# Kernel optimization log

Measured on AMD Instinct MI355X. Metric: run time of the kernel, lower is better.

The kernel has to match this reference:

```python
import jax, jax.numpy as jnp
import numpy as np

B, CIN, H, W = 1, 512, 128, 128
NC, D, P, NH = 10, 128, 200, 8
HW = H * W
DH = D // NH
FF = 256


def setup_inputs():
    key = jax.random.key(0)
    ks = jax.random.split(key, 20)
    def nrm(i, shape, s=0.02):
        return jax.random.normal(ks[i], shape, jnp.float32) * s
    # TransFusion create_2D_grid: pixel-center coords (x, y), flattened to [1, HW, 2]
    xs = jnp.arange(W, dtype=jnp.float32) + 0.5
    ys = jnp.arange(H, dtype=jnp.float32) + 0.5
    gx, gy = jnp.meshgrid(xs, ys, indexing='xy')
    bev_pos = jnp.stack([gx.reshape(-1), gy.reshape(-1)], axis=-1)[None]
    return {
        'x': jax.random.normal(ks[0], (B, CIN, H, W), jnp.float32),
        'w_shared': nrm(1, (D, CIN, 3, 3)), 'b_shared': jnp.zeros((D,), jnp.float32),
        'w_heat': nrm(2, (NC, D, 3, 3)), 'b_heat': jnp.full((NC,), -2.19, jnp.float32),
        'classes_eye': jnp.eye(NC, dtype=jnp.float32),
        'bev_pos': bev_pos,
        'w_ce': nrm(3, (D, NC)), 'b_ce': jnp.zeros((D,), jnp.float32),
        'w_qpos': nrm(4, (D, 2)), 'w_kpos': nrm(5, (D, 2)),
        'wq': nrm(6, (D, D)), 'wk': nrm(7, (D, D)), 'wv': nrm(8, (D, D)), 'wo': nrm(9, (D, D)),
        'ln1_g': jnp.ones((D,), jnp.float32), 'ln1_b': jnp.zeros((D,), jnp.float32),
        'ln2_g': jnp.ones((D,), jnp.float32), 'ln2_b': jnp.zeros((D,), jnp.float32),
        'w_ff1': nrm(10, (FF, D)), 'b_ff1': jnp.zeros((FF,), jnp.float32),
        'w_ff2': nrm(11, (D, FF)), 'b_ff2': jnp.zeros((D,), jnp.float32),
        'w_center': nrm(12, (2, D)), 'b_center': jnp.zeros((2,), jnp.float32),
        'w_height': nrm(13, (1, D)), 'b_height': jnp.zeros((1,), jnp.float32),
        'w_dim': nrm(14, (3, D)), 'b_dim': jnp.zeros((3,), jnp.float32),
        'w_rot': nrm(15, (2, D)), 'b_rot': jnp.zeros((2,), jnp.float32),
        'w_vel': nrm(16, (2, D)), 'b_vel': jnp.zeros((2,), jnp.float32),
        'w_hm': nrm(17, (NC, D)), 'b_hm': jnp.zeros((NC,), jnp.float32),
    }


def _conv2d(x, w, b):
    y = jax.lax.conv_general_dilated(x, w, (1, 1), 'SAME',
                                     dimension_numbers=('NCHW', 'OIHW', 'NCHW'))
    return y + b[None, :, None, None]


def _ln(x, g, b):
    m = jnp.mean(x, -1, keepdims=True)
    v = jnp.var(x, -1, keepdims=True)
    return (x - m) * jax.lax.rsqrt(v + 1e-5) * g + b


def reference(x, w_shared, b_shared, w_heat, b_heat, classes_eye, bev_pos,
              w_ce, b_ce, w_qpos, w_kpos, wq, wk, wv, wo,
              ln1_g, ln1_b, ln2_g, ln2_b, w_ff1, b_ff1, w_ff2, b_ff2,
              w_center, b_center, w_height, b_height, w_dim, b_dim,
              w_rot, b_rot, w_vel, b_vel, w_hm, b_hm):
    lidar_feat = jax.nn.relu(_conv2d(x, w_shared, b_shared))          # [B,D,H,W]
    lidar_flat = lidar_feat.reshape(B, D, HW)
    dense_heatmap = _conv2d(lidar_feat, w_heat, b_heat)               # [B,NC,H,W]
    heatmap = jax.lax.stop_gradient(jax.nn.sigmoid(dense_heatmap))    # .detach().sigmoid()
    # 3x3 local-max 'NMS'; zero-initialized border (F.max_pool2d VALID placed into zeros)
    inner = jax.lax.reduce_window(heatmap, -jnp.inf, jax.lax.max,
                                  (1, 1, 3, 3), (1, 1, 1, 1), 'VALID')
    local_max = jnp.zeros_like(heatmap).at[:, :, 1:-1, 1:-1].set(inner)
    local_max = local_max.at[:, 8].set(heatmap[:, 8])  # nuScenes: no NMS for cls 8,9
    local_max = local_max.at[:, 9].set(heatmap[:, 9])
    heatmap = heatmap * (heatmap == local_max)
    hm_flat = heatmap.reshape(B, NC, HW)
    # top-k proposals over flattened class*position axis
    _, top = jax.lax.top_k(hm_flat.reshape(B, -1), P)
    top_cls = top // HW                                               # [B,P]
    top_idx = top % HW                                                # [B,P]
    query_feat = jnp.take_along_axis(
        lidar_flat, jnp.broadcast_to(top_idx[:, None, :], (B, D, P)), axis=2)
    one_hot = classes_eye[top_cls].transpose(0, 2, 1)                 # [B,NC,P]
    # class encoding: 1x1 conv1d on one-hot
    query_feat = query_feat + jnp.einsum('dc,bcp->bdp', w_ce, one_hot) + b_ce[None, :, None]
    query_pos = jnp.take_along_axis(
        jnp.broadcast_to(bev_pos, (B, HW, 2)),
        jnp.broadcast_to(top_idx[:, :, None], (B, P, 2)), axis=1)     # [B,P,2]
    # single decoder layer: cross-attention of proposals over BEV features
    q_in = query_feat.transpose(0, 2, 1) + query_pos @ w_qpos.T       # [B,P,D]
    kv_in = lidar_flat.transpose(0, 2, 1) + bev_pos @ w_kpos.T        # [B,HW,D]
    q = (q_in @ wq.T).reshape(B, P, NH, DH)
    k = (kv_in @ wk.T).reshape(B, HW, NH, DH)
    v = (kv_in @ wv.T).reshape(B, HW, NH, DH)
    attn = jax.nn.softmax(jnp.einsum('bqhd,bkhd->bhqk', q, k) / np.sqrt(DH).astype(np.float32), axis=-1)
    out = jnp.einsum('bhqk,bkhd->bqhd', attn, v).reshape(B, P, D) @ wo.T
    h1 = _ln(query_feat.transpose(0, 2, 1) + out, ln1_g, ln1_b)
    ff = jax.nn.relu(h1 @ w_ff1.T + b_ff1) @ w_ff2.T + b_ff2
    h2 = _ln(h1 + ff, ln2_g, ln2_b)
    feat = h2.transpose(0, 2, 1)                                      # [B,D,P]
    def head(wt, bt):
        return jnp.einsum('od,bdp->bop', wt, feat) + bt[None, :, None]
    center = head(w_center, b_center) + query_pos.transpose(0, 2, 1)
    height = head(w_height, b_height)
    dim = head(w_dim, b_dim)
    rot = head(w_rot, b_rot)
    vel = head(w_vel, b_vel)
    hm_pred = head(w_hm, b_hm)
    query_heatmap_score = jnp.take_along_axis(
        hm_flat, jnp.broadcast_to(top_idx[:, None, :], (B, NC, P)), axis=2)
    # get_bboxes: sigmoid(heatmap) * query_heatmap_score * one_hot
    score = jax.nn.sigmoid(hm_pred) * query_heatmap_score * one_hot
    return (score, rot, dim, center, height, vel)
```

## Files before the change

### kernel.cpp

```cpp
#include <hip/hip_runtime.h>
#include <math.h>

#define HWSZ 16384

typedef __attribute__((ext_vector_type(8))) short short8;
typedef __attribute__((ext_vector_type(8))) unsigned short ush8;
typedef __attribute__((ext_vector_type(4))) float f4;
typedef __attribute__((ext_vector_type(16))) float f16x;

__device__ __forceinline__ ushort f2bf(float f) {
    unsigned u = __float_as_uint(f);
    return (ushort)((u + 0x7fffu + ((u >> 16) & 1u)) >> 16);
}
__device__ __forceinline__ float bf2f(ushort b) {
    return __uint_as_float(((unsigned)b) << 16);
}

__global__ void k_prep_w2(const float* __restrict__ w, float* __restrict__ wt) {
    int idx = blockIdx.x * 256 + threadIdx.x;
    if (idx >= 1152 * 16) return;
    int k = idx >> 4, oc = idx & 15;
    wt[idx] = (oc < 10) ? w[oc * 1152 + k] : 0.f;
}
__global__ void k_cvt_w(const float* __restrict__ w, ushort* __restrict__ wh,
                        ushort* __restrict__ wl) {
    int idx = blockIdx.x * 256 + threadIdx.x;
    if (idx >= 589824) return;
    int oc = idx / 4608, r = idx - oc * 4608;
    int tap = r >> 9, c = r & 511;
    float f = w[oc * 4608 + c * 9 + tap];
    ushort hb = f2bf(f);
    wh[idx] = hb;
    wl[idx] = f2bf(f - bf2f(hb));
}
__global__ void k_cvt_w128(const float* __restrict__ a, const float* __restrict__ b,
                           ushort* __restrict__ oa, ushort* __restrict__ ob) {
    int i = blockIdx.x * 256 + threadIdx.x;
    if (i < 16384) { oa[i] = f2bf(a[i]); ob[i] = f2bf(b[i]); }
}
__global__ __launch_bounds__(256) void k_cvt_x(const float* __restrict__ x,
        ushort* __restrict__ xh, ushort* __restrict__ xl) {
    __shared__ float T[64 * 65];
    int hw0 = blockIdx.x << 6;
    int c0 = blockIdx.y << 6;
    int t = threadIdx.x;
    {
        int cl = t >> 2, q = t & 3;
        const float* src = x + (size_t)(c0 + cl) * HWSZ + hw0 + q * 16;
        #pragma unroll
        for (int k = 0; k < 4; k++) {
            float4 v = *reinterpret_cast<const float4*>(src + k * 4);
            float* dst = &T[cl * 65 + q * 16 + k * 4];
            dst[0] = v.x; dst[1] = v.y; dst[2] = v.z; dst[3] = v.w;
        }
    }
    __syncthreads();
    {
        int hwl = t >> 2, q = t & 3;
        int cc = q * 16;
        size_t ob = (size_t)(hw0 + hwl) * 512 + c0 + cc;
        #pragma unroll
        for (int half = 0; half < 2; half++) {
            ush8 hv, lv;
            #pragma unroll
            for (int k = 0; k < 8; k++) {
                float f = T[(cc + half * 8 + k) * 65 + hwl];
                ushort hb = f2bf(f);
                hv[k] = hb;
                lv[k] = f2bf(f - bf2f(hb));
            }
            *reinterpret_cast<ush8*>(xh + ob + half * 8) = hv;
            *reinterpret_cast<ush8*>(xl + ob + half * 8) = lv;
        }
    }
}

__global__ __launch_bounds__(256) void k_conv1_mfma(
        const ushort* __restrict__ xh, const ushort* __restrict__ xl,
        const ushort* __restrict__ wh, const ushort* __restrict__ wl,
        const float* __restrict__ bias, float* __restrict__ out) {
    __shared__ ushort smem[30720];
    const int t = threadIdx.x;
    const int h = blockIdx.x >> 1, w0 = (blockIdx.x & 1) << 6;
    const int l = t & 63;
    const int wid = t >> 6;
    const int wm = wid >> 1, wn = wid & 1;
    const int l15 = l & 15, lhi = l >> 4;
    const int arow = t >> 2, achk = t & 3;

    f4 acc[2][4];
    #pragma unroll
    for (int m = 0; m < 2; m++)
        #pragma unroll
        for (int n = 0; n < 4; n++) acc[m][n] = (f4){0.f, 0.f, 0.f, 0.f};

    short8 rA[2], rB[2][2];
    const short8 zz = {0, 0, 0, 0, 0, 0, 0, 0};

    auto issue = [&](int it) {
        int c0 = (it / 9) << 5;
        int tap = it % 9;
        int dh = tap / 3 - 1, dw = tap % 3 - 1;
        int hh = h + dh;
        int wg = w0 + arow + dw;
        if (hh >= 0 && hh < 128 && wg >= 0 && wg < 128) {
            size_t off = ((size_t)(hh * 128 + wg) << 9) + c0 + (achk << 3);
            rA[0] = *reinterpret_cast<const short8*>(xh + off);
            rA[1] = *reinterpret_cast<const short8*>(xl + off);
        } else { rA[0] = zz; rA[1] = zz; }
        #pragma unroll
        for (int u = 0; u < 2; u++) {
            int oc = (u << 6) + (t >> 2);
            size_t off = (size_t)oc * 4608 + tap * 512 + c0 + (achk << 3);
            rB[u][0] = *reinterpret_cast<const short8*>(wh + off);
            rB[u][1] = *reinterpret_cast<const short8*>(wl + off);
        }
    };
    auto wstage = [&](int buf) {
        *reinterpret_cast<short8*>(&smem[buf * 5120 + arow * 40 + achk * 8]) = rA[0];
        *reinterpret_cast<short8*>(&smem[buf * 5120 + 2560 + arow * 40 + achk * 8]) = rA[1];
        #pragma unroll
        for (int u = 0; u < 2; u++) {
            int oc = (u << 6) + (t >> 2);
            *reinterpret_cast<short8*>(&smem[10240 + buf * 10240 + oc * 40 + achk * 8]) = rB[u][0];
            *reinterpret_cast<short8*>(&smem[10240 + buf * 10240 + 5120 + oc * 40 + achk * 8]) = rB[u][1];
        }
    };

    issue(0);
    wstage(0);
    issue(1);
    __syncthreads();

    for (int it = 0; it < 144; ++it) {
        int buf = it & 1;
        short8 aH[2], aL[2], bH[4], bL[4];
        #pragma unroll
        for (int m = 0; m < 2; m++) {
            int row = wm * 32 + m * 16 + l15;
            aH[m] = *reinterpret_cast<const short8*>(&smem[buf * 5120 + row * 40 + lhi * 8]);
            aL[m] = *reinterpret_cast<const short8*>(&smem[buf * 5120 + 2560 + row * 40 + lhi * 8]);
        }
        #pragma unroll
        for (int n = 0; n < 4; n++) {
            int oc = wn * 64 + n * 16 + l15;
            bH[n] = *reinterpret_cast<const short8*>(&smem[10240 + buf * 10240 + oc * 40 + lhi * 8]);
            bL[n] = *reinterpret_cast<const short8*>(&smem[10240 + buf * 10240 + 5120 + oc * 40 + lhi * 8]);
        }
        #pragma unroll
        for (int m = 0; m < 2; m++)
            #pragma unroll
            for (int n = 0; n < 4; n++) {
                acc[m][n] = __builtin_amdgcn_mfma_f32_16x16x32_bf16(aH[m], bH[n], acc[m][n], 0, 0, 0);
                acc[m][n] = __builtin_amdgcn_mfma_f32_16x16x32_bf16(aL[m], bH[n], acc[m][n], 0, 0, 0);
                acc[m][n] = __builtin_amdgcn_mfma_f32_16x16x32_bf16(aH[m], bL[n], acc[m][n], 0, 0, 0);
            }
        if (it + 1 < 144) {
            wstage(buf ^ 1);
            if (it + 2 < 144) issue(it + 2);
        }
        __syncthreads();
    }

    float* ot = reinterpret_cast<float*>(smem);
    #pragma unroll
    for (int m = 0; m < 2; m++)
        #pragma unroll
        for (int n = 0; n < 4; n++) {
            int oc = wn * 64 + n * 16 + l15;
            float b = bias[oc];
            #pragma unroll
            for (int r = 0; r < 4; r++) {
                int px = wm * 32 + m * 16 + lhi * 4 + r;
                ot[px * 132 + oc] = fmaxf(acc[m][n][r] + b, 0.f);
            }
        }
    __syncthreads();
    {
        int oc = t >> 1, half = t & 1;
        int base = h * 128 + w0 + half * 32;
        #pragma unroll
        for (int i = 0; i < 32; i += 4) {
            float4 v;
            v.x = ot[(half * 32 + i + 0) * 132 + oc];
            v.y = ot[(half * 32 + i + 1) * 132 + oc];
            v.z = ot[(half * 32 + i + 2) * 132 + oc];
            v.w = ot[(half * 32 + i + 3) * 132 + oc];
            *reinterpret_cast<float4*>(&out[(size_t)oc * HWSZ + base + i]) = v;
        }
    }
}

__global__ __launch_bounds__(256) void k_conv2(const float* __restrict__ lidar,
        const float* __restrict__ wt, const float* __restrict__ bias,
        float* __restrict__ sig) {
    __shared__ float xs[16 * 3 * 68];
    __shared__ float wsm[144 * 16];
    int bid = blockIdx.x;
    int h = bid >> 1, w0 = (bid & 1) << 6;
    int t = threadIdx.x;
    int tpx = (t & 15) << 2;
    int oc = t >> 4;
    float acc[4] = {0.f, 0.f, 0.f, 0.f};
    for (int c0 = 0; c0 < 128; c0 += 16) {
        for (int i = t; i < 16 * 3 * 66; i += 256) {
            int c = i / 198; int rem = i - c * 198; int r = rem / 66; int j = rem - r * 66;
            int gr = h - 1 + r, gc = w0 - 1 + j;
            float v = 0.f;
            if (((unsigned)gr < 128u) & ((unsigned)gc < 128u))
                v = lidar[(c0 + c) * HWSZ + gr * 128 + gc];
            xs[(c * 3 + r) * 68 + j] = v;
        }
        {
            const float4* src = (const float4*)(wt + c0 * 9 * 16);
            float4* dst = (float4*)wsm;
            for (int i = t; i < 576; i += 256) dst[i] = src[i];
        }
        __syncthreads();
        #pragma unroll 4
        for (int c = 0; c < 16; c++) {
            #pragma unroll
            for (int kh = 0; kh < 3; kh++) {
                const float* xr = &xs[(c * 3 + kh) * 68 + tpx];
                float xv0 = xr[0], xv1 = xr[1], xv2 = xr[2], xv3 = xr[3], xv4 = xr[4], xv5 = xr[5];
                #pragma unroll
                for (int kw = 0; kw < 3; kw++) {
                    float wv = wsm[(c * 9 + kh * 3 + kw) * 16 + oc];
                    float p0 = (kw == 0) ? xv0 : ((kw == 1) ? xv1 : xv2);
                    float p1 = (kw == 0) ? xv1 : ((kw == 1) ? xv2 : xv3);
                    float p2 = (kw == 0) ? xv2 : ((kw == 1) ? xv3 : xv4);
                    float p3 = (kw == 0) ? xv3 : ((kw == 1) ? xv4 : xv5);
                    acc[0] += p0 * wv; acc[1] += p1 * wv; acc[2] += p2 * wv; acc[3] += p3 * wv;
                }
            }
        }
        __syncthreads();
    }
    if (oc < 10) {
        float b = bias[oc];
        int col = h * 128 + w0 + tpx;
        float4 v;
        v.x = 1.f / (1.f + expf(-(acc[0] + b)));
        v.y = 1.f / (1.f + expf(-(acc[1] + b)));
        v.z = 1.f / (1.f + expf(-(acc[2] + b)));
        v.w = 1.f / (1.f + expf(-(acc[3] + b)));
        *(float4*)&sig[oc * HWSZ + col] = v;
    }
}

__global__ void k_nms(const float* __restrict__ sig, float* __restrict__ hm) {
    int gid = blockIdx.x * 256 + threadIdx.x;
    int c = gid >> 14, i = gid & 16383;
    int h = i >> 7, w = i & 127;
    float v = sig[gid];
    float keep = 0.f;
    if (c >= 8) keep = v;
    else if (h >= 1 && h <= 126 && w >= 1 && w <= 126) {
        const float* s = sig + c * HWSZ;
        float m = v;
        #pragma unroll
        for (int dh = -1; dh <= 1; dh++)
            #pragma unroll
            for (int dw = -1; dw <= 1; dw++)
                m = fmaxf(m, s[(h + dh) * 128 + (w + dw)]);
        keep = (v == m) ? v : 0.f;
    }
    hm[gid] = keep;
}

__global__ void k_hist_hi(const float* __restrict__ hm, unsigned* __restrict__ hist) {
    int gid = blockIdx.x * 256 + threadIdx.x;
    unsigned k = __float_as_uint(hm[gid]);
    if (k) atomicAdd(&hist[k >> 16], 1u);
}
__global__ void k_scan_hi(const unsigned* __restrict__ hist, unsigned* __restrict__ state) {
    __shared__ unsigned ps[256];
    __shared__ int selc;
    __shared__ unsigned selcum;
    __shared__ unsigned cb[256];
    int t = threadIdx.x;
    unsigned s = 0;
    const unsigned* hp = hist + t * 256;
    for (int i = 0; i < 256; i++) s += hp[i];
    ps[t] = s;
    __syncthreads();
    if (t == 0) {
        unsigned cum = 0; int c = 255;
        for (; c > 0; c--) { if (cum + ps[c] >= 200u) break; cum += ps[c]; }
        selc = c; selcum = cum;
    }
    __syncthreads();
    int c = selc;
    cb[t] = hist[c * 256 + t];
    __syncthreads();
    if (t == 0) {
        unsigned cum = selcum; int b = 255;
        for (; b > 0; b--) { if (cum + cb[b] >= 200u) break; cum += cb[b]; }
        state[8] = (unsigned)(c * 256 + b);
        state[9] = 200u - cum;
        state[10] = cum;
    }
}
__global__ void k_hist_lo(const float* __restrict__ hm, const unsigned* __restrict__ state,
                          unsigned* __restrict__ hist) {
    int gid = blockIdx.x * 256 + threadIdx.x;
    unsigned k = __float_as_uint(hm[gid]);
    if (k && (k >> 16) == state[8]) atomicAdd(&hist[k & 0xFFFFu], 1u);
}
__global__ void k_scan_lo(const unsigned* __restrict__ hist, unsigned* __restrict__ state) {
    __shared__ unsigned ps[256];
    __shared__ int selc;
    __shared__ unsigned selcum;
    __shared__ unsigned cb[256];
    int t = threadIdx.x;
    unsigned target = state[9];
    unsigned s = 0;
    const unsigned* hp = hist + t * 256;
    for (int i = 0; i < 256; i++) s += hp[i];
    ps[t] = s;
    __syncthreads();
    if (t == 0) {
        unsigned cum = 0; int c = 255;
        for (; c > 0; c--) { if (cum + ps[c] >= target) break; cum += ps[c]; }
        selc = c; selcum = cum;
    }
    __syncthreads();
    int c = selc;
    cb[t] = hist[c * 256 + t];
    __syncthreads();
    if (t == 0) {
        unsigned cum = selcum; int b = 255;
        for (; b > 0; b--) { if (cum + cb[b] >= target) break; cum += cb[b]; }
        unsigned lstar = (unsigned)(c * 256 + b);
        state[2] = (state[8] << 16) | lstar;
        state[0] = state[10] + cum;
        state[1] = target - cum;
    }
}
__global__ void k_collect(const float* __restrict__ hm, const unsigned* __restrict__ state,
        unsigned* __restrict__ ck, unsigned* __restrict__ ci,
        unsigned* __restrict__ ti, unsigned* __restrict__ cnts) {
    int gid = blockIdx.x * 256 + threadIdx.x;
    unsigned k = __float_as_uint(hm[gid]);
    unsigned ks = state[2];
    if (k > ks) {
        unsigned pos = atomicAdd(&cnts[0], 1u);
        if (pos < 256u) { ck[pos] = k; ci[pos] = (unsigned)gid; }
    } else if (k == ks) {
        unsigned pos = atomicAdd(&cnts[1], 1u);
        if (pos < 8192u) ti[pos] = (unsigned)gid;
    }
}
__global__ void k_topk_final(const unsigned* __restrict__ state, const unsigned* __restrict__ cnts,
        const unsigned* __restrict__ ck, const unsigned* __restrict__ ci,
        const unsigned* __restrict__ ti, int* __restrict__ top_pos, int* __restrict__ top_cls) {
    __shared__ unsigned kk[200], ii[200];
    int t = threadIdx.x;
    unsigned cgt = cnts[0];
    unsigned need = state[1];
    unsigned keystar = state[2];
    unsigned cntEq = cnts[1]; if (cntEq > 8192u) cntEq = 8192u;
    if ((unsigned)t < cgt && t < 200) { kk[t] = ck[t]; ii[t] = ci[t]; }
    for (unsigned e = t; e < cntEq; e += 256) {
        unsigned my = ti[e]; unsigned r = 0;
        for (unsigned j = 0; j < cntEq; j++) r += (ti[j] < my);
        if (r < need) { kk[cgt + r] = keystar; ii[cgt + r] = my; }
    }
    __syncthreads();
    if (t < 200) {
        unsigned mk = kk[t], mi = ii[t]; int r = 0;
        for (int j = 0; j < 200; j++) {
            unsigned ok = kk[j], oi = ii[j];
            r += (ok > mk) || (ok == mk && oi < mi);
        }
        top_cls[r] = (int)(mi >> 14);
        top_pos[r] = (int)(mi & 16383u);
    }
}

__global__ void k_gather(const float* __restrict__ lidar, const int* __restrict__ top_pos,
        const int* __restrict__ top_cls, const float* __restrict__ w_ce,
        const float* __restrict__ b_ce, const float* __restrict__ w_qpos,
        float* __restrict__ qf, float* __restrict__ qin, float* __restrict__ qpos) {
    int gid = blockIdx.x * 256 + threadIdx.x;
    if (gid >= 200 * 128) return;
    int p = gid >> 7, d = gid & 127;
    int idx = top_pos[p], cls = top_cls[p];
    float px = (float)(idx & 127) + 0.5f, py = (float)(idx >> 7) + 0.5f;
    float v = lidar[d * HWSZ + idx] + w_ce[d * 10 + cls] + b_ce[d];
    qf[gid] = v;
    qin[gid] = v + px * w_qpos[d * 2] + py * w_qpos[d * 2 + 1];
    if (d < 2) qpos[p * 2 + d] = (d == 0) ? px : py;
}

__global__ __launch_bounds__(256) void k_kvin(const float* __restrict__ lidar,
        const float* __restrict__ w_kpos, ushort* __restrict__ kv) {
    __shared__ float T[128 * 65];
    int hw0 = blockIdx.x << 6;
    int t = threadIdx.x;
    for (int i = t; i < 128 * 64; i += 256) {
        int d = i >> 6, c = i & 63;
        T[d * 65 + c] = lidar[d * HWSZ + hw0 + c];
    }
    __syncthreads();
    for (int i = t; i < 64 * 128; i += 256) {
        int r = i >> 7, d = i & 127;
        int hw = hw0 + r;
        float bx = (float)(hw & 127) + 0.5f, by = (float)(hw >> 7) + 0.5f;
        kv[(size_t)hw * 128 + d] = f2bf(T[d * 65 + r] + bx * w_kpos[d * 2] + by * w_kpos[d * 2 + 1]);
    }
}

__global__ __launch_bounds__(256) void k_gemm_kv(const ushort* __restrict__ A,
        const ushort* __restrict__ B, float* __restrict__ C) {
    __shared__ ushort As[64 * 136];
    __shared__ ushort Bs[128 * 136];
    int m0 = blockIdx.x << 6;
    int t = threadIdx.x;
    {
        int r = t >> 3, c = (t & 7) << 4;
        #pragma unroll
        for (int p = 0; p < 2; p++) {
            int row = p * 32 + r;
            const ush8* src = reinterpret_cast<const ush8*>(A + (size_t)(m0 + row) * 128 + c);
            *reinterpret_cast<ush8*>(&As[row * 136 + c]) = src[0];
            *reinterpret_cast<ush8*>(&As[row * 136 + c + 8]) = src[1];
        }
        #pragma unroll
        for (int p = 0; p < 4; p++) {
            int row = p * 32 + r;
            const ush8* src = reinterpret_cast<const ush8*>(B + (size_t)row * 128 + c);
            *reinterpret_cast<ush8*>(&Bs[row * 136 + c]) = src[0];
            *reinterpret_cast<ush8*>(&Bs[row * 136 + c + 8]) = src[1];
        }
    }
    __syncthreads();
    int l = t & 63, wid = t >> 6;
    int wm = wid >> 1, wn = wid & 1;
    int l31 = l & 31, lk = l >> 5;
    f16x acc[2];
    #pragma unroll
    for (int n = 0; n < 2; n++)
        #pragma unroll
        for (int i = 0; i < 16; i++) acc[n][i] = 0.f;
    #pragma unroll
    for (int ks = 0; ks < 8; ks++) {
        short8 aF = *reinterpret_cast<const short8*>(&As[(wm * 32 + l31) * 136 + ks * 16 + lk * 8]);
        #pragma unroll
        for (int n = 0; n < 2; n++) {
            short8 bF = *reinterpret_cast<const short8*>(&Bs[(wn * 64 + n * 32 + l31) * 136 + ks * 16 + lk * 8]);
            acc[n] = __builtin_amdgcn_mfma_f32_32x32x16_bf16(aF, bF, acc[n], 0, 0, 0);
        }
    }
    #pragma unroll
    for (int n = 0; n < 2; n++) {
        int oc = wn * 64 + n * 32 + l31;
        size_t cb = (size_t)(oc >> 4) * HWSZ * 16 + (oc & 15);
        #pragma unroll
        for (int r = 0; r < 16; r++) {
            int mrow = wm * 32 + (r & 3) + ((r >> 2) << 3) + (lk << 2);
            C[cb + (size_t)(m0 + mrow) * 16] = acc[n][r];
        }
    }
}

template<int EPI>
__global__ __launch_bounds__(256) void k_gemm(const float* __restrict__ A,
        const float* __restrict__ B, float* __restrict__ C, int M, int N, int K,
        const float* __restrict__ bias, const float* __restrict__ res) {
    __shared__ float As[16 * 68];
    __shared__ float Bs[16 * 68];
    int m0 = blockIdx.x * 64, n0 = blockIdx.y * 64;
    int t = threadIdx.x;
    int mi = (t & 15) << 2, ni = (t >> 4) << 2;
    float acc[4][4];
    #pragma unroll
    for (int i = 0; i < 4; i++)
        #pragma unroll
        for (int j = 0; j < 4; j++) acc[i][j] = 0.f;
    int r = t >> 2, kq = (t & 3) << 2;
    for (int k0 = 0; k0 < K; k0 += 16) {
        float4 v = make_float4(0.f, 0.f, 0.f, 0.f);
        if (m0 + r < M) v = *(const float4*)&A[(m0 + r) * K + k0 + kq];
        As[(kq + 0) * 68 + r] = v.x; As[(kq + 1) * 68 + r] = v.y;
        As[(kq + 2) * 68 + r] = v.z; As[(kq + 3) * 68 + r] = v.w;
        float4 w = *(const float4*)&B[(n0 + r) * K + k0 + kq];
        Bs[(kq + 0) * 68 + r] = w.x; Bs[(kq + 1) * 68 + r] = w.y;
        Bs[(kq + 2) * 68 + r] = w.z; Bs[(kq + 3) * 68 + r] = w.w;
        __syncthreads();
        #pragma unroll
        for (int k = 0; k < 16; k++) {
            float4 a = *(const float4*)&As[k * 68 + mi];
            float4 b = *(const float4*)&Bs[k * 68 + ni];
            acc[0][0] += a.x * b.x; acc[0][1] += a.x * b.y; acc[0][2] += a.x * b.z; acc[0][3] += a.x * b.w;
            acc[1][0] += a.y * b.x; acc[1][1] += a.y * b.y; acc[1][2] += a.y * b.z; acc[1][3] += a.y * b.w;
            acc[2][0] += a.z * b.x; acc[2][1] += a.z * b.y; acc[2][2] += a.z * b.z; acc[2][3] += a.z * b.w;
            acc[3][0] += a.w * b.x; acc[3][1] += a.w * b.y; acc[3][2] += a.w * b.z; acc[3][3] += a.w * b.w;
        }
        __syncthreads();
    }
    #pragma unroll
    for (int i = 0; i < 4; i++) {
        int m = m0 + mi + i;
        if (m >= M) continue;
        #pragma unroll
        for (int j = 0; j < 4; j++) {
            int n = n0 + ni + j;
            float v = acc[i][j];
            if (EPI == 2) v = fmaxf(v + bias[n], 0.f);
            if (EPI == 3) v += bias[n] + res[m * N + n];
            C[m * N + n] = v;
        }
    }
}

__global__ __launch_bounds__(256, 1) void k_attn_part(const float* __restrict__ Q,
        const float* __restrict__ Kp, const float* __restrict__ Vp,
        float* __restrict__ ps, float* __restrict__ pacc) {
    int head = blockIdx.y, chunk = blockIdx.z;
    int t = threadIdx.x;
    int wv = t >> 6, lane = t & 63;
    int qbase = (blockIdx.x * 4 + wv) * 4;
    float q[4][16];
    #pragma unroll
    for (int qq = 0; qq < 4; qq++) {
        int p = qbase + qq; if (p > 199) p = 199;
        const float4* qr = (const float4*)(Q + p * 128 + head * 16);
        #pragma unroll
        for (int u = 0; u < 4; u++) {
            float4 v = qr[u];
            q[qq][u * 4 + 0] = v.x * 0.25f; q[qq][u * 4 + 1] = v.y * 0.25f;
            q[qq][u * 4 + 2] = v.z * 0.25f; q[qq][u * 4 + 3] = v.w * 0.25f;
        }
    }
    const float* Kh = Kp + (size_t)head * HWSZ * 16;
    const float* Vh = Vp + (size_t)head * HWSZ * 16;
    float s[4] = {0.f, 0.f, 0.f, 0.f};
    float acc[4][16];
    #pragma unroll
    for (int qq = 0; qq < 4; qq++)
        #pragma unroll
        for (int i = 0; i < 16; i++) acc[qq][i] = 0.f;
    int k0 = chunk << 10;
    for (int kb = k0 + lane; kb < k0 + 1024; kb += 64) {
        const float4* kr = (const float4*)(Kh + (size_t)kb * 16);
        float4 ka = kr[0], kb4 = kr[1], kc = kr[2], kd = kr[3];
        float kk[16] = {ka.x, ka.y, ka.z, ka.w, kb4.x, kb4.y, kb4.z, kb4.w,
                        kc.x, kc.y, kc.z, kc.w, kd.x, kd.y, kd.z, kd.w};
        const float4* vr = (const float4*)(Vh + (size_t)kb * 16);
        float4 va = vr[0], vb = vr[1], vc = vr[2], vd = vr[3];
        float vv[16] = {va.x, va.y, va.z, va.w, vb.x, vb.y, vb.z, vb.w,
                        vc.x, vc.y, vc.z, vc.w, vd.x, vd.y, vd.z, vd.w};
        #pragma unroll
        for (int qq = 0; qq < 4; qq++) {
            float l0 = fmaf(q[qq][3], kk[3], fmaf(q[qq][2], kk[2], fmaf(q[qq][1], kk[1], q[qq][0] * kk[0])));
            float l1 = fmaf(q[qq][7], kk[7], fmaf(q[qq][6], kk[6], fmaf(q[qq][5], kk[5], q[qq][4] * kk[4])));
            float l2 = fmaf(q[qq][11], kk[11], fmaf(q[qq][10], kk[10], fmaf(q[qq][9], kk[9], q[qq][8] * kk[8])));
            float l3 = fmaf(q[qq][15], kk[15], fmaf(q[qq][14], kk[14], fmaf(q[qq][13], kk[13], q[qq][12] * kk[12])));
            float e = __expf((l0 + l1) + (l2 + l3));
            s[qq] += e;
            #pragma unroll
            for (int i = 0; i < 16; i++) acc[qq][i] = fmaf(e, vv[i], acc[qq][i]);
        }
    }
    #pragma unroll
    for (int mask = 32; mask >= 1; mask >>= 1) {
        #pragma unroll
        for (int qq = 0; qq < 4; qq++) {
            s[qq] += __shfl_xor(s[qq], mask);
            #pragma unroll
            for (int i = 0; i < 16; i++) acc[qq][i] += __shfl_xor(acc[qq][i], mask);
        }
    }
    if (lane == 0) {
        #pragma unroll
        for (int qq = 0; qq < 4; qq++) {
            int p = qbase + qq;
            int idx = (chunk * 8 + head) * 208 + p;
            ps[idx] = s[qq];
            #pragma unroll
            for (int i = 0; i < 16; i++) pacc[idx * 16 + i] = acc[qq][i];
        }
    }
}
__global__ __launch_bounds__(128) void k_attn_comb(const float* __restrict__ ps,
        const float* __restrict__ pacc, float* __restrict__ out) {
    int p = blockIdx.x;
    int t = threadIdx.x;
    int h = t >> 4, d = t & 15;
    float S = 0.f, A = 0.f;
    #pragma unroll
    for (int c = 0; c < 16; c++) {
        int idx = (c * 8 + h) * 208 + p;
        S += ps[idx];
        A += pacc[idx * 16 + d];
    }
    out[p * 128 + h * 16 + d] = A / S;
}

__global__ void k_ln(const float* __restrict__ a, const float* __restrict__ b,
        const float* __restrict__ g, const float* __restrict__ be, float* __restrict__ out) {
    int p = blockIdx.x, d = threadIdx.x;
    float x = a[p * 128 + d];
    if (b) x += b[p * 128 + d];
    __shared__ float red[4];
    float s = x;
    #pragma unroll
    for (int mask = 32; mask >= 1; mask >>= 1) s += __shfl_xor(s, mask);
    if ((d & 63) == 0) red[d >> 6] = s;
    __syncthreads();
    float mean = (red[0] + red[1]) * (1.f / 128.f);
    float dx = x - mean;
    float s2 = dx * dx;
    #pragma unroll
    for (int mask = 32; mask >= 1; mask >>= 1) s2 += __shfl_xor(s2, mask);
    if ((d & 63) == 0) red[2 + (d >> 6)] = s2;
    __syncthreads();
    float var = (red[2] + red[3]) * (1.f / 128.f);
    out[p * 128 + d] = dx * rsqrtf(var + 1e-5f) * g[d] + be[d];
}

__global__ void k_heads(const float* __restrict__ h2, const float* __restrict__ hm,
        const int* __restrict__ top_pos, const int* __restrict__ top_cls,
        const float* __restrict__ qpos,
        const float* __restrict__ w_hm, const float* __restrict__ b_hm,
        const float* __restrict__ w_rot, const float* __restrict__ b_rot,
        const float* __restrict__ w_dim, const float* __restrict__ b_dim,
        const float* __restrict__ w_center, const float* __restrict__ b_center,
        const float* __restrict__ w_height, const float* __restrict__ b_height,
        const float* __restrict__ w_vel, const float* __restrict__ b_vel,
        float* __restrict__ out) {
    int gid = blockIdx.x * 256 + threadIdx.x;
    if (gid >= 4000) return;
    int o = gid / 200, p = gid - o * 200;
    const float* wr; float bias;
    if (o < 10)      { wr = w_hm + o * 128;            bias = b_hm[o]; }
    else if (o < 12) { wr = w_rot + (o - 10) * 128;    bias = b_rot[o - 10]; }
    else if (o < 15) { wr = w_dim + (o - 12) * 128;    bias = b_dim[o - 12]; }
    else if (o < 17) { wr = w_center + (o - 15) * 128; bias = b_center[o - 15]; }
    else if (o < 18) { wr = w_height;                  bias = b_height[0]; }
    else             { wr = w_vel + (o - 18) * 128;    bias = b_vel[o - 18]; }
    const float* hr = h2 + p * 128;
    float dot = 0.f;
    #pragma unroll 8
    for (int d = 0; d < 128; d++) dot = fmaf(wr[d], hr[d], dot);
    dot += bias;
    float outv; int off;
    if (o < 10) {
        float qhs = hm[o * HWSZ + top_pos[p]];
        float oh = (top_cls[p] == o) ? 1.f : 0.f;
        outv = (1.f / (1.f + expf(-dot))) * qhs * oh;
        off = o * 200 + p;
    } else if (o < 12) { outv = dot; off = 2000 + (o - 10) * 200 + p; }
    else if (o < 15)   { outv = dot; off = 2400 + (o - 12) * 200 + p; }
    else if (o < 17)   { outv = dot + qpos[p * 2 + (o - 15)]; off = 3000 + (o - 15) * 200 + p; }
    else if (o < 18)   { outv = dot; off = 3400 + p; }
    else               { outv = dot; off = 3600 + (o - 18) * 200 + p; }
    out[off] = outv;
}

extern "C" void kernel_launch(void* const* d_in, const int* in_sizes, int n_in,
                              void* d_out, int out_size, void* d_ws, size_t ws_size,
                              hipStream_t stream) {
    const float* x        = (const float*)d_in[0];
    const float* w_shared = (const float*)d_in[1];
    const float* b_shared = (const float*)d_in[2];
    const float* w_heat   = (const float*)d_in[3];
    const float* b_heat   = (const float*)d_in[4];
    const float* w_ce     = (const float*)d_in[7];
    const float* b_ce     = (const float*)d_in[8];
    const float* w_qpos   = (const float*)d_in[9];
    const float* w_kpos   = (const float*)d_in[10];
    const float* wq       = (const float*)d_in[11];
    const float* wk       = (const float*)d_in[12];
    const float* wv       = (const float*)d_in[13];
    const float* wo       = (const float*)d_in[14];
    const float* ln1_g    = (const float*)d_in[15];
    const float* ln1_b    = (const float*)d_in[16];
    const float* ln2_g    = (const float*)d_in[17];
    const float* ln2_b    = (const float*)d_in[18];
    const float* w_ff1    = (const float*)d_in[19];
    const float* b_ff1    = (const float*)d_in[20];
    const float* w_ff2    = (const float*)d_in[21];
    const float* b_ff2    = (const float*)d_in[22];
    const float* w_center = (const float*)d_in[23];
    const float* b_center = (const float*)d_in[24];
    const float* w_height = (const float*)d_in[25];
    const float* b_height = (const float*)d_in[26];
    const float* w_dim    = (const float*)d_in[27];
    const float* b_dim    = (const float*)d_in[28];
    const float* w_rot    = (const float*)d_in[29];
    const float* b_rot    = (const float*)d_in[30];
    const float* w_vel    = (const float*)d_in[31];
    const float* b_vel    = (const float*)d_in[32];
    const float* w_hm     = (const float*)d_in[33];
    const float* b_hm     = (const float*)d_in[34];
    float* out = (float*)d_out;

    float* ws = (float*)d_ws;
    float* lidar = ws;
    float* bigR  = lidar + 2097152;
    ushort* xt_hi = (ushort*)bigR;
    ushort* xt_lo = xt_hi + 8388608;
    ushort* kvb  = (ushort*)bigR;
    float* KpB   = bigR + 2097152;
    float* VpB   = bigR + 4194304;
    float* wbh_f = bigR + 8388608;
    float* wbl_f = wbh_f + 294912;
    ushort* wb_hi = (ushort*)wbh_f;
    ushort* wb_lo = (ushort*)wbl_f;
    float* wt2   = wbl_f + 294912;
    float* sig   = wt2 + 18432;
    float* hmb   = sig + 163840;
    unsigned* hist_hi = (unsigned*)(hmb + 163840);
    unsigned* hist_lo = hist_hi + 65536;
    unsigned* state   = hist_lo + 65536;
    unsigned* cnts    = state + 64;
    unsigned* ck      = cnts + 64;
    unsigned* ci      = ck + 256;
    unsigned* ti      = ci + 256;
    int* top_pos      = (int*)(ti + 8192);
    int* top_cls      = top_pos + 256;
    float* qpos  = (float*)(top_cls + 256);
    float* qf    = qpos + 512;
    float* qin   = qf + 25600;
    float* qbuf  = qin + 25600;
    float* attno = qbuf + 25600;
    float* wo_o  = attno + 25600;
    float* h1    = wo_o + 25600;
    float* f1    = h1 + 25600;
    float* ff2o  = f1 + 51200;
    float* h2    = ff2o + 25600;
    float* ps_b  = h2 + 25600;
    float* pacc_b = ps_b + 26624;
    ushort* wkb  = (ushort*)(pacc_b + 425984);
    ushort* wvb  = wkb + 16384;
    size_t needed = (size_t)((pacc_b + 425984 + 16384) - ws) * sizeof(float);
    if (ws_size < needed) return;

    k_prep_w2<<<72, 256, 0, stream>>>(w_heat, wt2);
    k_cvt_w<<<2304, 256, 0, stream>>>(w_shared, wb_hi, wb_lo);
    k_cvt_w128<<<64, 256, 0, stream>>>(wk, wv, wkb, wvb);
    k_cvt_x<<<dim3(256, 8), 256, 0, stream>>>(x, xt_hi, xt_lo);
    k_conv1_mfma<<<256, 256, 0, stream>>>(xt_hi, xt_lo, wb_hi, wb_lo, b_shared, lidar);
    k_conv2<<<256, 256, 0, stream>>>(lidar, wt2, b_heat, sig);
    k_nms<<<640, 256, 0, stream>>>(sig, hmb);
    hipMemsetAsync(hist_hi, 0, (65536u * 2 + 128) * sizeof(unsigned), stream);
    k_hist_hi<<<640, 256, 0, stream>>>(hmb, hist_hi);
    k_scan_hi<<<1, 256, 0, stream>>>(hist_hi, state);
    k_hist_lo<<<640, 256, 0, stream>>>(hmb, state, hist_lo);
    k_scan_lo<<<1, 256, 0, stream>>>(hist_lo, state);
    k_collect<<<640, 256, 0, stream>>>(hmb, state, ck, ci, ti, cnts);
    k_topk_final<<<1, 256, 0, stream>>>(state, cnts, ck, ci, ti, top_pos, top_cls);
    k_gather<<<100, 256, 0, stream>>>(lidar, top_pos, top_cls, w_ce, b_ce, w_qpos, qf, qin, qpos);
    k_kvin<<<256, 256, 0, stream>>>(lidar, w_kpos, kvb);
    k_gemm<0><<<dim3(4, 2), 256, 0, stream>>>(qin, wq, qbuf, 200, 128, 128, nullptr, nullptr);
    k_gemm_kv<<<256, 256, 0, stream>>>(kvb, wkb, KpB);
    k_gemm_kv<<<256, 256, 0, stream>>>(kvb, wvb, VpB);
    k_attn_part<<<dim3(13, 8, 16), 256, 0, stream>>>(qbuf, KpB, VpB, ps_b, pacc_b);
    k_attn_comb<<<200, 128, 0, stream>>>(ps_b, pacc_b, attno);
    k_gemm<0><<<dim3(4, 2), 256, 0, stream>>>(attno, wo, wo_o, 200, 128, 128, nullptr, nullptr);
    k_ln<<<200, 128, 0, stream>>>(qf, wo_o, ln1_g, ln1_b, h1);
    k_gemm<2><<<dim3(4, 4), 256, 0, stream>>>(h1, w_ff1, f1, 200, 256, 128, b_ff1, nullptr);
    k_gemm<3><<<dim3(4, 2), 256, 0, stream>>>(f1, w_ff2, ff2o, 200, 128, 256, b_ff2, h1);
    k_ln<<<200, 128, 0, stream>>>(ff2o, nullptr, ln2_g, ln2_b, h2);
    k_heads<<<16, 256, 0, stream>>>(h2, hmb, top_pos, top_cls, qpos,
        w_hm, b_hm, w_rot, b_rot, w_dim, b_dim, w_center, b_center,
        w_height, b_height, w_vel, b_vel, out);
}
```

Measured before the change: 528.1 us.

## Fuse histogram into NMS, store K/V in bf16, fuse transformer tail

Three changes. The high-bits histogram atomics move into the NMS kernel, which drops one launch and one full reread of the heatmap. The K/V projection outputs are stored as bf16 instead of fp32, halving the bytes the attention kernel streams, at some precision cost. The Wo projection, LN1, FFN and LN2 are merged into one per-query kernel, replacing five small launches and their intermediate buffers with serial per-thread dot products.

```diff
diff --git a/kernel.cpp b/kernel.cpp
--- a/kernel.cpp
+++ b/kernel.cpp
@@ -248,7 +248,8 @@
     }
 }
 
-__global__ void k_nms(const float* __restrict__ sig, float* __restrict__ hm) {
+__global__ void k_nms(const float* __restrict__ sig, float* __restrict__ hm,
+                      unsigned* __restrict__ hist) {
     int gid = blockIdx.x * 256 + threadIdx.x;
     int c = gid >> 14, i = gid & 16383;
     int h = i >> 7, w = i & 127;
@@ -266,13 +267,10 @@
         keep = (v == m) ? v : 0.f;
     }
     hm[gid] = keep;
-}
-
-__global__ void k_hist_hi(const float* __restrict__ hm, unsigned* __restrict__ hist) {
-    int gid = blockIdx.x * 256 + threadIdx.x;
-    unsigned k = __float_as_uint(hm[gid]);
-    if (k) atomicAdd(&hist[k >> 16], 1u);
-}
+    unsigned kb = __float_as_uint(keep);
+    if (kb) atomicAdd(&hist[kb >> 16], 1u);
+}
+
 __global__ void k_scan_hi(const unsigned* __restrict__ hist, unsigned* __restrict__ state) {
     __shared__ unsigned ps[256];
     __shared__ int selc;
@@ -412,7 +410,7 @@
 }
 
 __global__ __launch_bounds__(256) void k_gemm_kv(const ushort* __restrict__ A,
-        const ushort* __restrict__ B, float* __restrict__ C) {
+        const ushort* __restrict__ B, ushort* __restrict__ C) {
     __shared__ ushort As[64 * 136];
     __shared__ ushort Bs[128 * 136];
     int m0 = blockIdx.x << 6;
@@ -459,7 +457,7 @@
         #pragma unroll
         for (int r = 0; r < 16; r++) {
             int mrow = wm * 32 + (r & 3) + ((r >> 2) << 3) + (lk << 2);
-            C[cb + (size_t)(m0 + mrow) * 16] = acc[n][r];
+            C[cb + (size_t)(m0 + mrow) * 16] = f2bf(acc[n][r]);
         }
     }
 }
@@ -515,7 +513,7 @@
 }
 
 __global__ __launch_bounds__(256, 1) void k_attn_part(const float* __restrict__ Q,
-        const float* __restrict__ Kp, const float* __restrict__ Vp,
+        const ushort* __restrict__ Kp, const ushort* __restrict__ Vp,
         float* __restrict__ ps, float* __restrict__ pacc) {
     int head = blockIdx.y, chunk = blockIdx.z;
     int t = threadIdx.x;
@@ -533,8 +531,8 @@
             q[qq][u * 4 + 2] = v.z * 0.25f; q[qq][u * 4 + 3] = v.w * 0.25f;
         }
     }
-    const float* Kh = Kp + (size_t)head * HWSZ * 16;
-    const float* Vh = Vp + (size_t)head * HWSZ * 16;
+    const ushort* Kh = Kp + (size_t)head * HWSZ * 16;
+    const ushort* Vh = Vp + (size_t)head * HWSZ * 16;
     float s[4] = {0.f, 0.f, 0.f, 0.f};
     float acc[4][16];
     #pragma unroll
@@ -543,14 +541,16 @@
         for (int i = 0; i < 16; i++) acc[qq][i] = 0.f;
     int k0 = chunk << 10;
     for (int kb = k0 + lane; kb < k0 + 1024; kb += 64) {
-        const float4* kr = (const float4*)(Kh + (size_t)kb * 16);
-        float4 ka = kr[0], kb4 = kr[1], kc = kr[2], kd = kr[3];
-        float kk[16] = {ka.x, ka.y, ka.z, ka.w, kb4.x, kb4.y, kb4.z, kb4.w,
-                        kc.x, kc.y, kc.z, kc.w, kd.x, kd.y, kd.z, kd.w};
-        const float4* vr = (const float4*)(Vh + (size_t)kb * 16);
-        float4 va = vr[0], vb = vr[1], vc = vr[2], vd = vr[3];
-        float vv[16] = {va.x, va.y, va.z, va.w, vb.x, vb.y, vb.z, vb.w,
-                        vc.x, vc.y, vc.z, vc.w, vd.x, vd.y, vd.z, vd.w};
+        const ush8* kr = reinterpret_cast<const ush8*>(Kh + (size_t)kb * 16);
+        ush8 kA = kr[0], kB = kr[1];
+        const ush8* vr = reinterpret_cast<const ush8*>(Vh + (size_t)kb * 16);
+        ush8 vA = vr[0], vB = vr[1];
+        float kk[16], vv[16];
+        #pragma unroll
+        for (int i = 0; i < 8; i++) {
+            kk[i] = bf2f(kA[i]); kk[8 + i] = bf2f(kB[i]);
+            vv[i] = bf2f(vA[i]); vv[8 + i] = bf2f(vB[i]);
+        }
         #pragma unroll
         for (int qq = 0; qq < 4; qq++) {
             float l0 = fmaf(q[qq][3], kk[3], fmaf(q[qq][2], kk[2], fmaf(q[qq][1], kk[1], q[qq][0] * kk[0])));
@@ -598,12 +598,22 @@
     out[p * 128 + h * 16 + d] = A / S;
 }
 
-__global__ void k_ln(const float* __restrict__ a, const float* __restrict__ b,
-        const float* __restrict__ g, const float* __restrict__ be, float* __restrict__ out) {
+__global__ __launch_bounds__(128) void k_tail(const float* __restrict__ attno,
+        const float* __restrict__ qf, const float* __restrict__ wo,
+        const float* __restrict__ ln1_g, const float* __restrict__ ln1_b,
+        const float* __restrict__ w_ff1, const float* __restrict__ b_ff1,
+        const float* __restrict__ w_ff2, const float* __restrict__ b_ff2,
+        const float* __restrict__ ln2_g, const float* __restrict__ ln2_b,
+        float* __restrict__ h2out) {
     int p = blockIdx.x, d = threadIdx.x;
-    float x = a[p * 128 + d];
-    if (b) x += b[p * 128 + d];
-    __shared__ float red[4];
+    __shared__ float att[128], h1s[128], fs[256], red[4];
+    att[d] = attno[p * 128 + d];
+    __syncthreads();
+    float acc = 0.f;
+    const float* wr = wo + d * 128;
+    #pragma unroll 8
+    for (int k = 0; k < 128; k++) acc = fmaf(wr[k], att[k], acc);
+    float x = qf[p * 128 + d] + acc;
     float s = x;
     #pragma unroll
     for (int mask = 32; mask >= 1; mask >>= 1) s += __shfl_xor(s, mask);
@@ -617,7 +627,41 @@
     if ((d & 63) == 0) red[2 + (d >> 6)] = s2;
     __syncthreads();
     float var = (red[2] + red[3]) * (1.f / 128.f);
-    out[p * 128 + d] = dx * rsqrtf(var + 1e-5f) * g[d] + be[d];
+    float h1v = dx * rsqrtf(var + 1e-5f) * ln1_g[d] + ln1_b[d];
+    h1s[d] = h1v;
+    __syncthreads();
+    float a0 = 0.f, a1 = 0.f;
+    const float* w1a = w_ff1 + d * 128;
+    const float* w1b = w_ff1 + (d + 128) * 128;
+    #pragma unroll 8
+    for (int k = 0; k < 128; k++) {
+        float hv = h1s[k];
+        a0 = fmaf(w1a[k], hv, a0);
+        a1 = fmaf(w1b[k], hv, a1);
+    }
+    fs[d] = fmaxf(a0 + b_ff1[d], 0.f);
+    fs[d + 128] = fmaxf(a1 + b_ff1[d + 128], 0.f);
+    __syncthreads();
+    float a2 = 0.f;
+    const float* w2 = w_ff2 + d * 256;
+    #pragma unroll 8
+    for (int j = 0; j < 256; j++) a2 = fmaf(w2[j], fs[j], a2);
+    float x2 = h1v + a2 + b_ff2[d];
+    __syncthreads();
+    float t2 = x2;
+    #pragma unroll
+    for (int mask = 32; mask >= 1; mask >>= 1) t2 += __shfl_xor(t2, mask);
+    if ((d & 63) == 0) red[d >> 6] = t2;
+    __syncthreads();
+    float mean2 = (red[0] + red[1]) * (1.f / 128.f);
+    float dx2 = x2 - mean2;
+    float v2 = dx2 * dx2;
+    #pragma unroll
+    for (int mask = 32; mask >= 1; mask >>= 1) v2 += __shfl_xor(v2, mask);
+    if ((d & 63) == 0) red[2 + (d >> 6)] = v2;
+    __syncthreads();
+    float var2 = (red[2] + red[3]) * (1.f / 128.f);
+    h2out[p * 128 + d] = dx2 * rsqrtf(var2 + 1e-5f) * ln2_g[d] + ln2_b[d];
 }
 
 __global__ void k_heads(const float* __restrict__ h2, const float* __restrict__ hm,
@@ -703,8 +747,8 @@
     ushort* xt_hi = (ushort*)bigR;
     ushort* xt_lo = xt_hi + 8388608;
     ushort* kvb  = (ushort*)bigR;
-    float* KpB   = bigR + 2097152;
-    float* VpB   = bigR + 4194304;
+    ushort* KpBh = (ushort*)(bigR + 1048576);
+    ushort* VpBh = (ushort*)(bigR + 2097152);
     float* wbh_f = bigR + 8388608;
     float* wbl_f = wbh_f + 294912;
     ushort* wb_hi = (ushort*)wbh_f;
@@ -726,11 +770,7 @@
     float* qin   = qf + 25600;
     float* qbuf  = qin + 25600;
     float* attno = qbuf + 25600;
-    float* wo_o  = attno + 25600;
-    float* h1    = wo_o + 25600;
-    float* f1    = h1 + 25600;
-    float* ff2o  = f1 + 51200;
-    float* h2    = ff2o + 25600;
+    float* h2    = attno + 25600;
     float* ps_b  = h2 + 25600;
     float* pacc_b = ps_b + 26624;
     ushort* wkb  = (ushort*)(pacc_b + 425984);
@@ -744,9 +784,8 @@
     k_cvt_x<<<dim3(256, 8), 256, 0, stream>>>(x, xt_hi, xt_lo);
     k_conv1_mfma<<<256, 256, 0, stream>>>(xt_hi, xt_lo, wb_hi, wb_lo, b_shared, lidar);
     k_conv2<<<256, 256, 0, stream>>>(lidar, wt2, b_heat, sig);
-    k_nms<<<640, 256, 0, stream>>>(sig, hmb);
     hipMemsetAsync(hist_hi, 0, (65536u * 2 + 128) * sizeof(unsigned), stream);
-    k_hist_hi<<<640, 256, 0, stream>>>(hmb, hist_hi);
+    k_nms<<<640, 256, 0, stream>>>(sig, hmb, hist_hi);
     k_scan_hi<<<1, 256, 0, stream>>>(hist_hi, state);
     k_hist_lo<<<640, 256, 0, stream>>>(hmb, state, hist_lo);
     k_scan_lo<<<1, 256, 0, stream>>>(hist_lo, state);
@@ -755,15 +794,12 @@
     k_gather<<<100, 256, 0, stream>>>(lidar, top_pos, top_cls, w_ce, b_ce, w_qpos, qf, qin, qpos);
     k_kvin<<<256, 256, 0, stream>>>(lidar, w_kpos, kvb);
     k_gemm<0><<<dim3(4, 2), 256, 0, stream>>>(qin, wq, qbuf, 200, 128, 128, nullptr, nullptr);
-    k_gemm_kv<<<256, 256, 0, stream>>>(kvb, wkb, KpB);
-    k_gemm_kv<<<256, 256, 0, stream>>>(kvb, wvb, VpB);
-    k_attn_part<<<dim3(13, 8, 16), 256, 0, stream>>>(qbuf, KpB, VpB, ps_b, pacc_b);
+    k_gemm_kv<<<256, 256, 0, stream>>>(kvb, wkb, KpBh);
+    k_gemm_kv<<<256, 256, 0, stream>>>(kvb, wvb, VpBh);
+    k_attn_part<<<dim3(13, 8, 16), 256, 0, stream>>>(qbuf, KpBh, VpBh, ps_b, pacc_b);
     k_attn_comb<<<200, 128, 0, stream>>>(ps_b, pacc_b, attno);
-    k_gemm<0><<<dim3(4, 2), 256, 0, stream>>>(attno, wo, wo_o, 200, 128, 128, nullptr, nullptr);
-    k_ln<<<200, 128, 0, stream>>>(qf, wo_o, ln1_g, ln1_b, h1);
-    k_gemm<2><<<dim3(4, 4), 256, 0, stream>>>(h1, w_ff1, f1, 200, 256, 128, b_ff1, nullptr);
-    k_gemm<3><<<dim3(4, 2), 256, 0, stream>>>(f1, w_ff2, ff2o, 200, 128, 256, b_ff2, h1);
-    k_ln<<<200, 128, 0, stream>>>(ff2o, nullptr, ln2_g, ln2_b, h2);
+    k_tail<<<200, 128, 0, stream>>>(attno, qf, wo, ln1_g, ln1_b,
+        w_ff1, b_ff1, w_ff2, b_ff2, ln2_g, ln2_b, h2);
     k_heads<<<16, 256, 0, stream>>>(h2, hmb, top_pos, top_cls, qpos,
         w_hm, b_hm, w_rot, b_rot, w_dim, b_dim, w_center, b_center,
         w_height, b_height, w_vel, b_vel, out);
```

New measurement: 496.7 us. -5.9%, faster.
